# Kernel tuning notes

Hardware: AMD Instinct MI355X
Metric: run time of the kernel (lower is better)

Reference implementation:

```python
import jax, jax.numpy as jnp
import numpy as np

T, B, H = 256, 64, 1024

def setup_inputs() -> dict:
    key = jax.random.key(0)
    k0, k1, k2, k3 = jax.random.split(key, 4)
    x = jax.random.normal(k0, (T, B, H), dtype=jnp.float32)
    # episode resets are sparse events
    resets = jax.random.bernoulli(k1, 0.01, (T, B))
    h0 = jnp.zeros((B, H), dtype=jnp.float32)  # flax GRUCell.initialize_carry -> zeros
    s = np.float32(1.0 / np.sqrt(H))
    Wi = jax.random.normal(k2, (H, 3 * H), dtype=jnp.float32) * s  # packed [ir|iz|in]
    Wh = jax.random.normal(k3, (H, 3 * H), dtype=jnp.float32) * s  # packed [hr|hz|hn]
    bi = jnp.zeros((3 * H,), dtype=jnp.float32)
    bn = jnp.zeros((H,), dtype=jnp.float32)  # only the 'n' hidden dense has a bias in flax
    return dict(x=x, resets=resets, h0=h0, Wi=Wi, bi=bi, Wh=Wh, bn=bn)

def reference(x, resets, h0, Wi, bi, Wh, bn):
    """Scanned GRU with reset masking, matching flax nn.scan(GRUCell)."""
    def step(h, inp):
        x_t, r_t = inp  # [B,H], [B]
        h = jnp.where(r_t[:, None], jnp.zeros_like(h), h)  # reset carry to initial (zeros)
        gi = x_t @ Wi + bi          # [B,3H]
        gh = h @ Wh                 # [B,3H]
        ir, iz, inn = jnp.split(gi, 3, axis=-1)
        hr, hz, hn = jnp.split(gh, 3, axis=-1)
        r = jax.nn.sigmoid(ir + hr)
        z = jax.nn.sigmoid(iz + hz)
        n = jnp.tanh(inn + r * (hn + bn))
        h_new = (1.0 - z) * n + z * h
        return h_new, h_new  # GRUCell returns (new_state, y=new_state)
    h_final, ys = jax.lax.scan(step, h0, (x, resets))
    return h_final, ys
```

## Files before the change

### kernel.cpp

```cpp
#include <hip/hip_runtime.h>
#include <hip/hip_bf16.h>
#include <cstdint>


#define TT 256
#define BB 64
#define HH 1024
#define H3 3072

typedef __attribute__((ext_vector_type(8))) short s16x8;
typedef __attribute__((ext_vector_type(4))) float f32x4;
typedef __attribute__((ext_vector_type(4))) unsigned int u32x4;
typedef unsigned long long ull;

__device__ __forceinline__ float fast_sigmoid(float x) {
  float e = __expf(-fabsf(x));
  float s = 1.0f / (1.0f + e);
  return x >= 0.0f ? s : 1.0f - s;
}
__device__ __forceinline__ float fast_tanh(float x) {
  float e = __expf(-2.0f * fabsf(x));
  float t = (1.0f - e) / (1.0f + e);
  return x >= 0.0f ? t : -t;
}
__device__ __forceinline__ f32x4 mfma16(s16x8 a, s16x8 b, f32x4 c) {
  return __builtin_amdgcn_mfma_f32_16x16x32_bf16(a, b, c, 0, 0, 0);
}

#define LD8(p) __hip_atomic_load((p), __ATOMIC_RELAXED, __HIP_MEMORY_SCOPE_AGENT)
#define ST8(p, v) __hip_atomic_store((p), (v), __ATOMIC_RELAXED, __HIP_MEMORY_SCOPE_AGENT)


__global__ void k_cvt_x(const float* __restrict__ x, __hip_bfloat16* __restrict__ xb, int n) {
  int i = (blockIdx.x * blockDim.x + threadIdx.x) * 4;
  if (i + 3 < n) {
    float4 v = *reinterpret_cast<const float4*>(x + i);
    xb[i + 0] = __float2bfloat16(v.x);
    xb[i + 1] = __float2bfloat16(v.y);
    xb[i + 2] = __float2bfloat16(v.z);
    xb[i + 3] = __float2bfloat16(v.w);
  }
}

__global__ void k_transpose_w(const float* __restrict__ W, __hip_bfloat16* __restrict__ WT) {
  __shared__ float tile[32][33];
  int c0 = blockIdx.x * 32, r0 = blockIdx.y * 32;
  int tx = threadIdx.x & 31, ty = threadIdx.x >> 5;
#pragma unroll
  for (int i = 0; i < 32; i += 8)
    tile[ty + i][tx] = W[(size_t)(r0 + ty + i) * H3 + c0 + tx];
  __syncthreads();
#pragma unroll
  for (int i = 0; i < 32; i += 8)
    WT[(size_t)(c0 + ty + i) * HH + r0 + tx] = __float2bfloat16(tile[tx][ty + i]);
}


template <bool GIF32>
__global__ __launch_bounds__(256, 2) void k_gemm_gi(
    const __hip_bfloat16* __restrict__ A,
    const __hip_bfloat16* __restrict__ Bt,
    const float* __restrict__ bi,
    void* __restrict__ gi)
{
  __shared__ __align__(16) __hip_bfloat16 As[128 * 32];
  __shared__ __align__(16) __hip_bfloat16 Bs[128 * 32];
  const int bid = blockIdx.x;
  const int mt = bid / 24, nt = bid % 24;
  const int m0 = mt * 128, n0 = nt * 128;
  const int tid = threadIdx.x, lane = tid & 63, w = tid >> 6;
  const int wm = w & 1, wn = w >> 1;

  f32x4 acc[4][4];
#pragma unroll
  for (int ai = 0; ai < 4; ++ai)
#pragma unroll
    for (int bj = 0; bj < 4; ++bj) acc[ai][bj] = (f32x4){0.f, 0.f, 0.f, 0.f};

  for (int k0 = 0; k0 < HH; k0 += 32) {
#pragma unroll
    for (int i = 0; i < 2; ++i) {
      const int c = w + i * 4;
      const int idx = c * 64 + lane;
      const int row = idx >> 2, slot = idx & 3;
      __builtin_amdgcn_global_load_lds(
          (const __attribute__((address_space(1))) void*)(A + (size_t)(m0 + row) * HH + k0 + slot * 8),
          (__attribute__((address_space(3))) void*)(As + c * 512), 16, 0, 0);
      __builtin_amdgcn_global_load_lds(
          (const __attribute__((address_space(1))) void*)(Bt + (size_t)(n0 + row) * HH + k0 + slot * 8),
          (__attribute__((address_space(3))) void*)(Bs + c * 512), 16, 0, 0);
    }
    __syncthreads();
    s16x8 af[4], bf[4];
#pragma unroll
    for (int ai = 0; ai < 4; ++ai) {
      int r = wm * 64 + ai * 16 + (lane & 15);
      af[ai] = *reinterpret_cast<const s16x8*>(As + r * 32 + (lane >> 4) * 8);
    }
#pragma unroll
    for (int bj = 0; bj < 4; ++bj) {
      int r = wn * 64 + bj * 16 + (lane & 15);
      bf[bj] = *reinterpret_cast<const s16x8*>(Bs + r * 32 + (lane >> 4) * 8);
    }
#pragma unroll
    for (int ai = 0; ai < 4; ++ai)
#pragma unroll
      for (int bj = 0; bj < 4; ++bj) acc[ai][bj] = mfma16(af[ai], bf[bj], acc[ai][bj]);
    __syncthreads();
  }

#pragma unroll
  for (int ai = 0; ai < 4; ++ai) {
#pragma unroll
    for (int reg = 0; reg < 4; ++reg) {
      const size_t row = (size_t)m0 + wm * 64 + ai * 16 + (lane >> 4) * 4 + reg;
#pragma unroll
      for (int bj = 0; bj < 4; ++bj) {
        const int col = n0 + wn * 64 + bj * 16 + (lane & 15);
        float v = acc[ai][bj][reg] + bi[col];
        if (GIF32)
          reinterpret_cast<float*>(gi)[row * H3 + col] = v;
        else
          reinterpret_cast<__hip_bfloat16*>(gi)[row * H3 + col] = __float2bfloat16(v);
      }
    }
  }
}


template <bool GIF32>
__global__ __launch_bounds__(256, 1) void k_gru(
    const void* __restrict__ gi_,
    const int* __restrict__ resets,
    const float* __restrict__ h0,
    const float* __restrict__ bn,
    const __hip_bfloat16* __restrict__ WhT,
    __hip_bfloat16* hseq,
    float* __restrict__ out)
{
  __shared__ __align__(16) __hip_bfloat16 Bsh[48 * 1024];
  __shared__ __align__(16) f32x4 part[2][4][3][64];
  __shared__ __align__(8) __hip_bfloat16 hsh[16][16];
  const int tid = threadIdx.x;
  const int wave = tid >> 6, lane = tid & 63;
  const int wg = blockIdx.x;
  const int g = (wg & 7) >> 1;
  const int s = ((wg >> 3) << 1) | (wg & 1);
  const int bg0 = g * 16, j0 = s * 16;

  for (int cch = tid; cch < 48 * 128; cch += 256) {
    const int row = cch >> 7, slot = cch & 127;
    const int gate = row >> 4, jj = row & 15;
    u32x4 v = *reinterpret_cast<const u32x4*>(WhT + (size_t)(gate * HH + j0 + jj) * HH + slot * 8);
    const int byte = row * 2048 + ((slot * 16) ^ ((row & 7) << 4));
    *reinterpret_cast<u32x4*>(reinterpret_cast<char*>(Bsh) + byte) = v;
  }

  const int bl = tid >> 4;
  const int jl = tid & 15;
  const int b = bg0 + bl, j = j0 + jl;
  const float bnj = bn[j];
  float hp = h0[(size_t)b * HH + j];
  int rstE;
  float giR, giZ, giN;
  {
    rstE = resets[b];
    if (GIF32) {
      const float* grow = reinterpret_cast<const float*>(gi_) + (size_t)b * H3;
      giR = grow[j]; giZ = grow[HH + j]; giN = grow[2 * HH + j];
    } else {
      const __hip_bfloat16* grow = reinterpret_cast<const __hip_bfloat16*>(gi_) + (size_t)b * H3;
      giR = __bfloat162float(grow[j]);
      giZ = __bfloat162float(grow[HH + j]);
      giN = __bfloat162float(grow[2 * HH + j]);
    }
  }

  hsh[bl][jl] = __float2bfloat16(hp);
  __syncthreads();
  if (lane < 16) {
    const int prow = wave * 4 + (lane >> 2), pq = (lane & 3) * 4;
    ull pv = *reinterpret_cast<const ull*>(&hsh[prow][pq]);
    ST8(reinterpret_cast<ull*>(hseq + (size_t)g * 16384 + prow * HH + j0 + pq), pv);
  }

  const int al = lane & 15;
  const int koff = (lane >> 4) * 8;
  const char* bbase = reinterpret_cast<const char*>(Bsh);
  const int xsw = (jl & 7) << 4;
  const int rb0 = jl * 2048, rb1 = (16 + jl) * 2048, rb2 = (32 + jl) * 2048;
  const int cprod = lane & 15, crow = (lane >> 4) * 4 + 1;

  for (int t = 0; t < TT; ++t) {
    const int rstA = resets[t * BB + bg0 + al];
    const __hip_bfloat16* rd = hseq + (size_t)t * 65536 + g * 16384;

    {
      const ull* cp = reinterpret_cast<const ull*>(rd + crow * HH + wave * 256 + cprod * 16 + 8);
      int gq = 0;
      ull c;
      do {
        c = LD8(cp);
      } while (__any((int)(c == ~0ull)) && ++gq < (1 << 20));
    }

    const ull* ch = reinterpret_cast<const ull*>(rd + al * HH + koff) + wave * 64;
    ull w[16];
#pragma unroll
    for (int i = 0; i < 8; ++i) {
      w[2 * i + 0] = LD8(ch + i * 8 + 0);
      w[2 * i + 1] = LD8(ch + i * 8 + 1);
    }
    {
      int gq = 0;
      for (;;) {
        unsigned bad = 0;
#pragma unroll
        for (int i = 0; i < 16; ++i) bad |= (unsigned)(w[i] == ~0ull);
        if (!__any((int)bad) || ++gq >= (1 << 18)) break;
#pragma unroll
        for (int i = 0; i < 8; ++i) {
          w[2 * i + 0] = LD8(ch + i * 8 + 0);
          w[2 * i + 1] = LD8(ch + i * 8 + 1);
        }
      }
    }

    const ull amask = rstA ? 0ull : ~0ull;
    f32x4 aR = {0.f, 0.f, 0.f, 0.f}, aZ = {0.f, 0.f, 0.f, 0.f}, aN = {0.f, 0.f, 0.f, 0.f};
#pragma unroll
    for (int i = 0; i < 8; ++i) {
      const int kk = wave * 8 + i;
      union { ull q[2]; s16x8 v; } u;
      u.q[0] = w[2 * i + 0] & amask;
      u.q[1] = w[2 * i + 1] & amask;
      const int kb = kk * 64 + (lane >> 4) * 16;
      s16x8 b0 = *reinterpret_cast<const s16x8*>(bbase + rb0 + (kb ^ xsw));
      s16x8 b1 = *reinterpret_cast<const s16x8*>(bbase + rb1 + (kb ^ xsw));
      s16x8 b2 = *reinterpret_cast<const s16x8*>(bbase + rb2 + (kb ^ xsw));
      aR = mfma16(u.v, b0, aR);
      aZ = mfma16(u.v, b1, aZ);
      aN = mfma16(u.v, b2, aN);
    }

    const int p = t & 1;
    part[p][wave][0][lane] = aR;
    part[p][wave][1][lane] = aZ;
    part[p][wave][2][lane] = aN;
    __syncthreads();

    const int li = ((bl >> 2) << 4) | jl, el = bl & 3;
    float sR = part[p][0][0][li][el], sZ = part[p][0][1][li][el], sN = part[p][0][2][li][el];
#pragma unroll
    for (int ww = 1; ww < 4; ++ww) {
      sR += part[p][ww][0][li][el];
      sZ += part[p][ww][1][li][el];
      sN += part[p][ww][2][li][el];
    }
    const float hprev = rstE ? 0.f : hp;
    const float rg = fast_sigmoid(giR + sR);
    const float zg = fast_sigmoid(giZ + sZ);
    const float ng = fast_tanh(giN + rg * (sN + bnj));
    const float hnew = (1.0f - zg) * ng + zg * hprev;
    hp = hnew;

    hsh[bl][jl] = __float2bfloat16(hnew);
    if (lane < 16) {
      const int prow = wave * 4 + (lane >> 2), pq = (lane & 3) * 4;
      ull pv = *reinterpret_cast<const ull*>(&hsh[prow][pq]);
      ST8(reinterpret_cast<ull*>(hseq + (size_t)(t + 1) * 65536 + g * 16384 + prow * HH + j0 + pq),
          pv);
    }

    __builtin_nontemporal_store(hnew, out + 65536 + (size_t)t * 65536 + (size_t)b * HH + j);

    const int tn = (t + 1 < TT) ? t + 1 : t;
    rstE = resets[tn * BB + b];
    if (GIF32) {
      const float* grow = reinterpret_cast<const float*>(gi_) + (size_t)(tn * BB + b) * H3;
      giR = grow[j]; giZ = grow[HH + j]; giN = grow[2 * HH + j];
    } else {
      const __hip_bfloat16* grow =
          reinterpret_cast<const __hip_bfloat16*>(gi_) + (size_t)(tn * BB + b) * H3;
      giR = __bfloat162float(grow[j]);
      giZ = __bfloat162float(grow[HH + j]);
      giN = __bfloat162float(grow[2 * HH + j]);
    }
  }

  out[(size_t)b * HH + j] = hp;
}


extern "C" void kernel_launch(void* const* d_in, const int* in_sizes, int n_in,
                              void* d_out, int out_size, void* d_ws, size_t ws_size,
                              hipStream_t stream) {
  const float* x      = (const float*)d_in[0];
  const int* resets   = (const int*)d_in[1];
  const float* h0     = (const float*)d_in[2];
  const float* Wi     = (const float*)d_in[3];
  const float* bi     = (const float*)d_in[4];
  const float* Wh     = (const float*)d_in[5];
  const float* bn     = (const float*)d_in[6];
  (void)in_sizes; (void)n_in; (void)out_size;

  char* ws = (char*)d_ws;
  __hip_bfloat16* xb   = (__hip_bfloat16*)(ws);
  __hip_bfloat16* hseq = (__hip_bfloat16*)(ws);
  __hip_bfloat16* WiT  = (__hip_bfloat16*)(ws + 33685504);
  __hip_bfloat16* WhT  = (__hip_bfloat16*)(ws + 39976960);
  void* gi             = (void*)(ws + 46268416);

  const bool gif32 = ws_size >= 46268416ull + (size_t)16384 * 3072 * 4;

  k_cvt_x<<<16384, 256, 0, stream>>>(x, xb, TT * BB * HH);
  k_transpose_w<<<dim3(96, 32), 256, 0, stream>>>(Wi, WiT);
  k_transpose_w<<<dim3(96, 32), 256, 0, stream>>>(Wh, WhT);
  if (gif32) {
    k_gemm_gi<true><<<3072, 256, 0, stream>>>(xb, WiT, bi, gi);
    hipMemsetAsync(hseq, 0xFF, 33685504, stream);
    k_gru<true><<<256, 256, 0, stream>>>(gi, resets, h0, bn, WhT, hseq, (float*)d_out);
  } else {
    k_gemm_gi<false><<<3072, 256, 0, stream>>>(xb, WiT, bi, gi);
    hipMemsetAsync(hseq, 0xFF, 33685504, stream);
    k_gru<false><<<256, 256, 0, stream>>>(gi, resets, h0, bn, WhT, hseq, (float*)d_out);
  }
}
```

Before: 1.283 ms.

## Prefetch next step's hidden state speculatively and drop the separate canary poll

Measured after the change: 1.649 ms. 1.29x slower.

```diff
diff --git a/kernel.cpp b/kernel.cpp
--- a/kernel.cpp
+++ b/kernel.cpp
@@ -127,6 +127,103 @@
   }
 }
 
+
+#define ISSUE16(W, CH)                                   \
+  do {                                                   \
+    _Pragma("unroll") for (int i_ = 0; i_ < 8; ++i_) {   \
+      W[2 * i_ + 0] = LD8((CH) + i_ * 8 + 0);            \
+      W[2 * i_ + 1] = LD8((CH) + i_ * 8 + 1);            \
+    }                                                    \
+  } while (0)
+
+#define VERIFY16(W, CH)                                                      \
+  do {                                                                       \
+    int gq_ = 0;                                                             \
+    for (;;) {                                                               \
+      unsigned bad_ = 0;                                                     \
+      _Pragma("unroll") for (int i_ = 0; i_ < 16; ++i_)                      \
+          bad_ |= (unsigned)(W[i_] == ~0ull);                                \
+      if (!__any((int)bad_) || ++gq_ >= (1 << 18)) break;                    \
+      ISSUE16(W, CH);                                                        \
+    }                                                                        \
+  } while (0)
+
+#define STEP(T, CUR, NXT)                                                     \
+  do {                                                                        \
+    const int t_ = (T);                                                       \
+    const ull* ch_ =                                                          \
+        reinterpret_cast<const ull*>(hseq + (size_t)t_ * 65536 + g * 16384 +  \
+                                     al * HH + koff) + wave * 64;             \
+    const int rstA_ = resets[t_ * BB + bg0 + al];                             \
+    VERIFY16(CUR, ch_);                                                       \
+    const ull amask_ = rstA_ ? 0ull : ~0ull;                                  \
+    f32x4 aR_ = {0.f, 0.f, 0.f, 0.f}, aZ_ = {0.f, 0.f, 0.f, 0.f},             \
+          aN_ = {0.f, 0.f, 0.f, 0.f};                                         \
+    _Pragma("unroll") for (int i_ = 0; i_ < 8; ++i_) {                        \
+      const int kk_ = wave * 8 + i_;                                          \
+      union { ull q[2]; s16x8 v; } u_;                                        \
+      u_.q[0] = CUR[2 * i_ + 0] & amask_;                                     \
+      u_.q[1] = CUR[2 * i_ + 1] & amask_;                                     \
+      const int kb_ = kk_ * 64 + (lane >> 4) * 16;                            \
+      s16x8 b0_ = *reinterpret_cast<const s16x8*>(bbase + rb0 + (kb_ ^ xsw)); \
+      s16x8 b1_ = *reinterpret_cast<const s16x8*>(bbase + rb1 + (kb_ ^ xsw)); \
+      s16x8 b2_ = *reinterpret_cast<const s16x8*>(bbase + rb2 + (kb_ ^ xsw)); \
+      aR_ = mfma16(u_.v, b0_, aR_);                                           \
+      aZ_ = mfma16(u_.v, b1_, aZ_);                                           \
+      aN_ = mfma16(u_.v, b2_, aN_);                                           \
+    }                                                                         \
+    const int p_ = t_ & 1;                                                    \
+    part[p_][wave][0][lane] = aR_;                                            \
+    part[p_][wave][1][lane] = aZ_;                                            \
+    part[p_][wave][2][lane] = aN_;                                            \
+    __syncthreads();                                                          \
+    const int li_ = ((bl >> 2) << 4) | jl, el_ = bl & 3;                      \
+    float sR_ = part[p_][0][0][li_][el_], sZ_ = part[p_][0][1][li_][el_],     \
+          sN_ = part[p_][0][2][li_][el_];                                     \
+    _Pragma("unroll") for (int ww_ = 1; ww_ < 4; ++ww_) {                     \
+      sR_ += part[p_][ww_][0][li_][el_];                                      \
+      sZ_ += part[p_][ww_][1][li_][el_];                                      \
+      sN_ += part[p_][ww_][2][li_][el_];                                      \
+    }                                                                         \
+    const float hprev_ = rstE ? 0.f : hp;                                     \
+    const float rg_ = fast_sigmoid(giR + sR_);                                \
+    const float zg_ = fast_sigmoid(giZ + sZ_);                                \
+    const float ng_ = fast_tanh(giN + rg_ * (sN_ + bnj));                     \
+    const float hnew_ = (1.0f - zg_) * ng_ + zg_ * hprev_;                    \
+    hp = hnew_;                                                               \
+        \
+    hsh[bl][jl] = __float2bfloat16(hnew_);                                    \
+    if (lane < 16) {                                                          \
+      const int prow_ = wave * 4 + (lane >> 2), pq_ = (lane & 3) * 4;         \
+      ull pv_ = *reinterpret_cast<const ull*>(&hsh[prow_][pq_]);              \
+      ST8(reinterpret_cast<ull*>(hseq + (size_t)(t_ + 1) * 65536 +            \
+                                 g * 16384 + prow_ * HH + j0 + pq_),          \
+          pv_);                                                               \
+    }                                                                         \
+     \
+    const ull* chn_ =                                                         \
+        reinterpret_cast<const ull*>(hseq + (size_t)(t_ + 1) * 65536 +        \
+                                     g * 16384 + al * HH + koff) + wave * 64; \
+    ISSUE16(NXT, chn_);                                                       \
+                               \
+    __builtin_nontemporal_store(                                              \
+        hp, out + 65536 + (size_t)t_ * 65536 + (size_t)b * HH + j);           \
+                                         \
+    const int tn_ = (t_ + 1 < TT) ? t_ + 1 : t_;                              \
+    rstE = resets[tn_ * BB + b];                                              \
+    if (GIF32) {                                                              \
+      const float* grow_ =                                                    \
+          reinterpret_cast<const float*>(gi_) + (size_t)(tn_ * BB + b) * H3;  \
+      giR = grow_[j]; giZ = grow_[HH + j]; giN = grow_[2 * HH + j];           \
+    } else {                                                                  \
+      const __hip_bfloat16* grow_ =                                           \
+          reinterpret_cast<const __hip_bfloat16*>(gi_) +                      \
+          (size_t)(tn_ * BB + b) * H3;                                        \
+      giR = __bfloat162float(grow_[j]);                                       \
+      giZ = __bfloat162float(grow_[HH + j]);                                  \
+      giN = __bfloat162float(grow_[2 * HH + j]);                              \
+    }                                                                         \
+  } while (0)
 
 template <bool GIF32>
 __global__ __launch_bounds__(256, 1) void k_gru(
@@ -189,103 +286,17 @@
   const char* bbase = reinterpret_cast<const char*>(Bsh);
   const int xsw = (jl & 7) << 4;
   const int rb0 = jl * 2048, rb1 = (16 + jl) * 2048, rb2 = (32 + jl) * 2048;
-  const int cprod = lane & 15, crow = (lane >> 4) * 4 + 1;
-
-  for (int t = 0; t < TT; ++t) {
-    const int rstA = resets[t * BB + bg0 + al];
-    const __hip_bfloat16* rd = hseq + (size_t)t * 65536 + g * 16384;
-
-    {
-      const ull* cp = reinterpret_cast<const ull*>(rd + crow * HH + wave * 256 + cprod * 16 + 8);
-      int gq = 0;
-      ull c;
-      do {
-        c = LD8(cp);
-      } while (__any((int)(c == ~0ull)) && ++gq < (1 << 20));
-    }
-
-    const ull* ch = reinterpret_cast<const ull*>(rd + al * HH + koff) + wave * 64;
-    ull w[16];
-#pragma unroll
-    for (int i = 0; i < 8; ++i) {
-      w[2 * i + 0] = LD8(ch + i * 8 + 0);
-      w[2 * i + 1] = LD8(ch + i * 8 + 1);
-    }
-    {
-      int gq = 0;
-      for (;;) {
-        unsigned bad = 0;
-#pragma unroll
-        for (int i = 0; i < 16; ++i) bad |= (unsigned)(w[i] == ~0ull);
-        if (!__any((int)bad) || ++gq >= (1 << 18)) break;
-#pragma unroll
-        for (int i = 0; i < 8; ++i) {
-          w[2 * i + 0] = LD8(ch + i * 8 + 0);
-          w[2 * i + 1] = LD8(ch + i * 8 + 1);
-        }
-      }
-    }
-
-    const ull amask = rstA ? 0ull : ~0ull;
-    f32x4 aR = {0.f, 0.f, 0.f, 0.f}, aZ = {0.f, 0.f, 0.f, 0.f}, aN = {0.f, 0.f, 0.f, 0.f};
-#pragma unroll
-    for (int i = 0; i < 8; ++i) {
-      const int kk = wave * 8 + i;
-      union { ull q[2]; s16x8 v; } u;
-      u.q[0] = w[2 * i + 0] & amask;
-      u.q[1] = w[2 * i + 1] & amask;
-      const int kb = kk * 64 + (lane >> 4) * 16;
-      s16x8 b0 = *reinterpret_cast<const s16x8*>(bbase + rb0 + (kb ^ xsw));
-      s16x8 b1 = *reinterpret_cast<const s16x8*>(bbase + rb1 + (kb ^ xsw));
-      s16x8 b2 = *reinterpret_cast<const s16x8*>(bbase + rb2 + (kb ^ xsw));
-      aR = mfma16(u.v, b0, aR);
-      aZ = mfma16(u.v, b1, aZ);
-      aN = mfma16(u.v, b2, aN);
-    }
-
-    const int p = t & 1;
-    part[p][wave][0][lane] = aR;
-    part[p][wave][1][lane] = aZ;
-    part[p][wave][2][lane] = aN;
-    __syncthreads();
-
-    const int li = ((bl >> 2) << 4) | jl, el = bl & 3;
-    float sR = part[p][0][0][li][el], sZ = part[p][0][1][li][el], sN = part[p][0][2][li][el];
-#pragma unroll
-    for (int ww = 1; ww < 4; ++ww) {
-      sR += part[p][ww][0][li][el];
-      sZ += part[p][ww][1][li][el];
-      sN += part[p][ww][2][li][el];
-    }
-    const float hprev = rstE ? 0.f : hp;
-    const float rg = fast_sigmoid(giR + sR);
-    const float zg = fast_sigmoid(giZ + sZ);
-    const float ng = fast_tanh(giN + rg * (sN + bnj));
-    const float hnew = (1.0f - zg) * ng + zg * hprev;
-    hp = hnew;
-
-    hsh[bl][jl] = __float2bfloat16(hnew);
-    if (lane < 16) {
-      const int prow = wave * 4 + (lane >> 2), pq = (lane & 3) * 4;
-      ull pv = *reinterpret_cast<const ull*>(&hsh[prow][pq]);
-      ST8(reinterpret_cast<ull*>(hseq + (size_t)(t + 1) * 65536 + g * 16384 + prow * HH + j0 + pq),
-          pv);
-    }
-
-    __builtin_nontemporal_store(hnew, out + 65536 + (size_t)t * 65536 + (size_t)b * HH + j);
-
-    const int tn = (t + 1 < TT) ? t + 1 : t;
-    rstE = resets[tn * BB + b];
-    if (GIF32) {
-      const float* grow = reinterpret_cast<const float*>(gi_) + (size_t)(tn * BB + b) * H3;
-      giR = grow[j]; giZ = grow[HH + j]; giN = grow[2 * HH + j];
-    } else {
-      const __hip_bfloat16* grow =
-          reinterpret_cast<const __hip_bfloat16*>(gi_) + (size_t)(tn * BB + b) * H3;
-      giR = __bfloat162float(grow[j]);
-      giZ = __bfloat162float(grow[HH + j]);
-      giN = __bfloat162float(grow[2 * HH + j]);
-    }
+
+  ull wA[16], wB[16];
+  {
+    const ull* ch0 =
+        reinterpret_cast<const ull*>(hseq + (size_t)g * 16384 + al * HH + koff) + wave * 64;
+    ISSUE16(wA, ch0);
+  }
+
+  for (int t = 0; t < TT; t += 2) {
+    STEP(t, wA, wB);
+    STEP(t + 1, wB, wA);
   }
 
   out[(size_t)b * HH + j] = hp;
```

## Retile GRU recurrence to 8 batch rows by 32 hidden units, N-gate weights in registers

Applied to the files above, without the earlier changes.

New measurement: 1.302 ms. About the same (+1.5%).

```diff
diff --git a/kernel.cpp b/kernel.cpp
--- a/kernel.cpp
+++ b/kernel.cpp
@@ -29,6 +29,14 @@
 
 #define LD8(p) __hip_atomic_load((p), __ATOMIC_RELAXED, __HIP_MEMORY_SCOPE_AGENT)
 #define ST8(p, v) __hip_atomic_store((p), (v), __ATOMIC_RELAXED, __HIP_MEMORY_SCOPE_AGENT)
+
+__device__ __forceinline__ u32x4 ld16_opaque(const char* p) {
+  u32x4 r;
+  asm volatile("global_load_dwordx4 %0, %1, off\n\t"
+               "s_waitcnt vmcnt(0)"
+               : "=&v"(r) : "v"(p) : "memory");
+  return r;
+}
 
 
 __global__ void k_cvt_x(const float* __restrict__ x, __hip_bfloat16* __restrict__ xb, int n) {
@@ -138,65 +146,73 @@
     __hip_bfloat16* hseq,
     float* __restrict__ out)
 {
-  __shared__ __align__(16) __hip_bfloat16 Bsh[48 * 1024];
-  __shared__ __align__(16) f32x4 part[2][4][3][64];
-  __shared__ __align__(8) __hip_bfloat16 hsh[16][16];
+  __shared__ __align__(16) char Wlds[64 * 2048];
+  __shared__ __align__(16) f32x4 part[2][4][6][32];
+  __shared__ __align__(8) __hip_bfloat16 hsh[8][32];
+
   const int tid = threadIdx.x;
   const int wave = tid >> 6, lane = tid & 63;
   const int wg = blockIdx.x;
-  const int g = (wg & 7) >> 1;
-  const int s = ((wg >> 3) << 1) | (wg & 1);
-  const int bg0 = g * 16, j0 = s * 16;
-
-  for (int cch = tid; cch < 48 * 128; cch += 256) {
-    const int row = cch >> 7, slot = cch & 127;
-    const int gate = row >> 4, jj = row & 15;
-    u32x4 v = *reinterpret_cast<const u32x4*>(WhT + (size_t)(gate * HH + j0 + jj) * HH + slot * 8);
-    const int byte = row * 2048 + ((slot * 16) ^ ((row & 7) << 4));
-    *reinterpret_cast<u32x4*>(reinterpret_cast<char*>(Bsh) + byte) = v;
-  }
-
-  const int bl = tid >> 4;
-  const int jl = tid & 15;
+  const int g = wg & 7, s = wg >> 3;
+  const int bg0 = g * 8, j0 = s * 32;
+  const int l15 = lane & 15;
+
+  const int bl = tid >> 5;
+  const int jl = tid & 31;
   const int b = bg0 + bl, j = j0 + jl;
   const float bnj = bn[j];
   float hp = h0[(size_t)b * HH + j];
-  int rstE;
+
+  hsh[bl][jl] = __float2bfloat16(hp);
+  if (lane < 16) {
+    const int prow = wave * 2 + (lane >> 3);
+    const int pw = lane & 7;
+    ull pv = *reinterpret_cast<const ull*>(&hsh[prow][pw * 4]);
+    ST8(reinterpret_cast<ull*>(hseq + (size_t)(bg0 + prow) * HH + j0 + pw * 4), pv);
+  }
+
+  for (int u = tid; u < 64 * 128; u += 256) {
+    const int row = u >> 7, sl = u & 127;
+    const int gate = row >> 5, jj = row & 31;
+    u32x4 v = *reinterpret_cast<const u32x4*>(WhT + (size_t)(gate * HH + j0 + jj) * HH + sl * 8);
+    const int byte = row * 2048 + ((sl * 16) ^ ((row & 7) << 4));
+    *reinterpret_cast<u32x4*>(Wlds + byte) = v;
+  }
+
+  u32x4 bnf[16];
+#pragma unroll
+  for (int nt = 0; nt < 2; ++nt)
+#pragma unroll
+    for (int kk = 0; kk < 8; ++kk)
+      bnf[nt * 8 + kk] = ld16_opaque(reinterpret_cast<const char*>(
+          WhT + (size_t)(2 * HH + j0 + nt * 16 + l15) * HH + wave * 256 + kk * 32 + (lane >> 4) * 8));
+
+  int rstE = resets[b];
   float giR, giZ, giN;
-  {
-    rstE = resets[b];
-    if (GIF32) {
-      const float* grow = reinterpret_cast<const float*>(gi_) + (size_t)b * H3;
-      giR = grow[j]; giZ = grow[HH + j]; giN = grow[2 * HH + j];
-    } else {
-      const __hip_bfloat16* grow = reinterpret_cast<const __hip_bfloat16*>(gi_) + (size_t)b * H3;
-      giR = __bfloat162float(grow[j]);
-      giZ = __bfloat162float(grow[HH + j]);
-      giN = __bfloat162float(grow[2 * HH + j]);
-    }
-  }
-
-  hsh[bl][jl] = __float2bfloat16(hp);
+  if (GIF32) {
+    const float* grow = reinterpret_cast<const float*>(gi_) + (size_t)b * H3;
+    giR = grow[j]; giZ = grow[HH + j]; giN = grow[2 * HH + j];
+  } else {
+    const __hip_bfloat16* grow = reinterpret_cast<const __hip_bfloat16*>(gi_) + (size_t)b * H3;
+    giR = __bfloat162float(grow[j]);
+    giZ = __bfloat162float(grow[HH + j]);
+    giN = __bfloat162float(grow[2 * HH + j]);
+  }
+
+  const int alr = lane & 7;
+  const int koff = (lane >> 4) * 8;
+  const int cprod = lane >> 3, crow = lane & 7;
+  const size_t cansub = (size_t)(bg0 + crow) * HH + (wave * 8 + cprod) * 32 + 28;
+
   __syncthreads();
-  if (lane < 16) {
-    const int prow = wave * 4 + (lane >> 2), pq = (lane & 3) * 4;
-    ull pv = *reinterpret_cast<const ull*>(&hsh[prow][pq]);
-    ST8(reinterpret_cast<ull*>(hseq + (size_t)g * 16384 + prow * HH + j0 + pq), pv);
-  }
-
-  const int al = lane & 15;
-  const int koff = (lane >> 4) * 8;
-  const char* bbase = reinterpret_cast<const char*>(Bsh);
-  const int xsw = (jl & 7) << 4;
-  const int rb0 = jl * 2048, rb1 = (16 + jl) * 2048, rb2 = (32 + jl) * 2048;
-  const int cprod = lane & 15, crow = (lane >> 4) * 4 + 1;
 
   for (int t = 0; t < TT; ++t) {
-    const int rstA = resets[t * BB + bg0 + al];
-    const __hip_bfloat16* rd = hseq + (size_t)t * 65536 + g * 16384;
+    const int p = t & 1;
+    const int rstA = resets[t * BB + bg0 + alr];
+    const __hip_bfloat16* rd = hseq + (size_t)t * 65536;
 
     {
-      const ull* cp = reinterpret_cast<const ull*>(rd + crow * HH + wave * 256 + cprod * 16 + 8);
+      const ull* cp = reinterpret_cast<const ull*>(rd + cansub);
       int gq = 0;
       ull c;
       do {
@@ -204,12 +220,13 @@
       } while (__any((int)(c == ~0ull)) && ++gq < (1 << 20));
     }
 
-    const ull* ch = reinterpret_cast<const ull*>(rd + al * HH + koff) + wave * 64;
+    const ull* ch = reinterpret_cast<const ull*>(
+        rd + (size_t)(bg0 + alr) * HH + wave * 256 + koff);
     ull w[16];
 #pragma unroll
-    for (int i = 0; i < 8; ++i) {
-      w[2 * i + 0] = LD8(ch + i * 8 + 0);
-      w[2 * i + 1] = LD8(ch + i * 8 + 1);
+    for (int kk = 0; kk < 8; ++kk) {
+      w[2 * kk + 0] = LD8(ch + kk * 8 + 0);
+      w[2 * kk + 1] = LD8(ch + kk * 8 + 1);
     }
     {
       int gq = 0;
@@ -219,43 +236,50 @@
         for (int i = 0; i < 16; ++i) bad |= (unsigned)(w[i] == ~0ull);
         if (!__any((int)bad) || ++gq >= (1 << 18)) break;
 #pragma unroll
-        for (int i = 0; i < 8; ++i) {
-          w[2 * i + 0] = LD8(ch + i * 8 + 0);
-          w[2 * i + 1] = LD8(ch + i * 8 + 1);
+        for (int kk = 0; kk < 8; ++kk) {
+          w[2 * kk + 0] = LD8(ch + kk * 8 + 0);
+          w[2 * kk + 1] = LD8(ch + kk * 8 + 1);
         }
       }
     }
 
-    const ull amask = rstA ? 0ull : ~0ull;
-    f32x4 aR = {0.f, 0.f, 0.f, 0.f}, aZ = {0.f, 0.f, 0.f, 0.f}, aN = {0.f, 0.f, 0.f, 0.f};
-#pragma unroll
-    for (int i = 0; i < 8; ++i) {
-      const int kk = wave * 8 + i;
+    const ull amask = ((l15 < 8) && !rstA) ? ~0ull : 0ull;
+    f32x4 acc[6];
+#pragma unroll
+    for (int tl = 0; tl < 6; ++tl) acc[tl] = (f32x4){0.f, 0.f, 0.f, 0.f};
+#pragma unroll
+    for (int kk = 0; kk < 8; ++kk) {
       union { ull q[2]; s16x8 v; } u;
-      u.q[0] = w[2 * i + 0] & amask;
-      u.q[1] = w[2 * i + 1] & amask;
-      const int kb = kk * 64 + (lane >> 4) * 16;
-      s16x8 b0 = *reinterpret_cast<const s16x8*>(bbase + rb0 + (kb ^ xsw));
-      s16x8 b1 = *reinterpret_cast<const s16x8*>(bbase + rb1 + (kb ^ xsw));
-      s16x8 b2 = *reinterpret_cast<const s16x8*>(bbase + rb2 + (kb ^ xsw));
-      aR = mfma16(u.v, b0, aR);
-      aZ = mfma16(u.v, b1, aZ);
-      aN = mfma16(u.v, b2, aN);
-    }
-
-    const int p = t & 1;
-    part[p][wave][0][lane] = aR;
-    part[p][wave][1][lane] = aZ;
-    part[p][wave][2][lane] = aN;
+      u.q[0] = w[2 * kk + 0] & amask;
+      u.q[1] = w[2 * kk + 1] & amask;
+      const int kb = wave * 512 + kk * 64 + (lane >> 4) * 16;
+#pragma unroll
+      for (int nt = 0; nt < 2; ++nt) {
+        const int rR = nt * 16 + l15;
+        const int rZ = 32 + nt * 16 + l15;
+        s16x8 br = *reinterpret_cast<const s16x8*>(Wlds + rR * 2048 + (kb ^ ((rR & 7) << 4)));
+        s16x8 bz = *reinterpret_cast<const s16x8*>(Wlds + rZ * 2048 + (kb ^ ((rZ & 7) << 4)));
+        acc[0 + nt] = mfma16(u.v, br, acc[0 + nt]);
+        acc[2 + nt] = mfma16(u.v, bz, acc[2 + nt]);
+        acc[4 + nt] = mfma16(u.v, __builtin_bit_cast(s16x8, bnf[nt * 8 + kk]), acc[4 + nt]);
+      }
+    }
+    if (lane < 32) {
+#pragma unroll
+      for (int tl = 0; tl < 6; ++tl) part[p][wave][tl][lane] = acc[tl];
+    }
     __syncthreads();
 
-    const int li = ((bl >> 2) << 4) | jl, el = bl & 3;
-    float sR = part[p][0][0][li][el], sZ = part[p][0][1][li][el], sN = part[p][0][2][li][el];
+    const int nt = jl >> 4;
+    const int li = ((bl >> 2) << 4) | (jl & 15), el = bl & 3;
+    float sR = part[p][0][0 + nt][li][el];
+    float sZ = part[p][0][2 + nt][li][el];
+    float sN = part[p][0][4 + nt][li][el];
 #pragma unroll
     for (int ww = 1; ww < 4; ++ww) {
-      sR += part[p][ww][0][li][el];
-      sZ += part[p][ww][1][li][el];
-      sN += part[p][ww][2][li][el];
+      sR += part[p][ww][0 + nt][li][el];
+      sZ += part[p][ww][2 + nt][li][el];
+      sN += part[p][ww][4 + nt][li][el];
     }
     const float hprev = rstE ? 0.f : hp;
     const float rg = fast_sigmoid(giR + sR);
@@ -266,9 +290,11 @@
 
     hsh[bl][jl] = __float2bfloat16(hnew);
     if (lane < 16) {
-      const int prow = wave * 4 + (lane >> 2), pq = (lane & 3) * 4;
-      ull pv = *reinterpret_cast<const ull*>(&hsh[prow][pq]);
-      ST8(reinterpret_cast<ull*>(hseq + (size_t)(t + 1) * 65536 + g * 16384 + prow * HH + j0 + pq),
+      const int prow = wave * 2 + (lane >> 3);
+      const int pw = lane & 7;
+      ull pv = *reinterpret_cast<const ull*>(&hsh[prow][pw * 4]);
+      ST8(reinterpret_cast<ull*>(hseq + (size_t)(t + 1) * 65536 +
+                                 (size_t)(bg0 + prow) * HH + j0 + pw * 4),
           pv);
     }
 
```
